# Optimization experiments

Hardware: AMD Instinct MI355X
Metric: run time of the kernel (lower is better)

The kernel has to match this reference:

```python
import jax, jax.numpy as jnp
import numpy as np

NUM_LAYERS = 10
HIDDEN = 5
INPUT = 5
SEQ = 457
OUT = 457


def _lstm_layer(x_tbi, W_ih, W_hh, b):
    # x_tbi: [T, B, in]; W_ih: [4H, in]; W_hh: [4H, H]; b: [4H] (b_ih + b_hh)
    B = x_tbi.shape[1]
    h0 = jnp.zeros((B, HIDDEN), x_tbi.dtype)
    c0 = jnp.zeros((B, HIDDEN), x_tbi.dtype)
    # precompute input projections for all timesteps: [T, B, 4H]
    xW = jnp.einsum('tbi,gi->tbg', x_tbi, W_ih) + b

    def step(carry, xw_t):
        h, c = carry
        gates = xw_t + h @ W_hh.T  # [B, 4H]
        i, f, g, o = jnp.split(gates, 4, axis=-1)  # PyTorch gate order i,f,g,o
        i = jax.nn.sigmoid(i)
        f = jax.nn.sigmoid(f)
        g = jnp.tanh(g)
        o = jax.nn.sigmoid(o)
        c = f * c + i * g
        h = o * jnp.tanh(c)
        return (h, c), h

    (_, _), hs = jax.lax.scan(step, (h0, c0), xW)
    return hs  # [T, B, H]


def setup_inputs() -> dict:
    key = jax.random.key(0)
    ks = jax.random.split(key, 8)
    B = 4096
    x = jax.random.normal(ks[0], (B, SEQ, INPUT), dtype=jnp.float32)
    attn = jnp.ones((B, SEQ), dtype=jnp.int64)
    tok = jnp.zeros((B, SEQ), dtype=jnp.int64)
    s = 1.0 / np.sqrt(HIDDEN)
    # layer 0 input size == HIDDEN, so all layers stack uniformly
    W_ih = jax.random.uniform(ks[1], (NUM_LAYERS, 4 * HIDDEN, INPUT), jnp.float32, -s, s)
    W_hh = jax.random.uniform(ks[2], (NUM_LAYERS, 4 * HIDDEN, HIDDEN), jnp.float32, -s, s)
    b_ih = jax.random.uniform(ks[3], (NUM_LAYERS, 4 * HIDDEN), jnp.float32, -s, s)
    b_hh = jax.random.uniform(ks[4], (NUM_LAYERS, 4 * HIDDEN), jnp.float32, -s, s)
    sf = 1.0 / np.sqrt(HIDDEN * SEQ)
    fc_W = jax.random.uniform(ks[5], (OUT, HIDDEN * SEQ), jnp.float32, -sf, sf)
    fc_b = jax.random.uniform(ks[6], (OUT,), jnp.float32, -sf, sf)
    return {"a_input_ids": x, "a_attention_mask": attn, "a_token_type_ids": tok,
            "W_ih": W_ih, "W_hh": W_hh, "b_ih": b_ih, "b_hh": b_hh,
            "fc_W": fc_W, "fc_b": fc_b}


def reference(a_input_ids, a_attention_mask, a_token_type_ids, W_ih, W_hh, b_ih, b_hh, fc_W, fc_b):
    x = jnp.transpose(a_input_ids.astype(jnp.float32), (1, 0, 2))  # [T, B, 5]
    b = b_ih + b_hh
    for l in range(NUM_LAYERS):
        x = _lstm_layer(x, W_ih[l], W_hh[l], b[l])  # [T, B, H]
    out = jnp.transpose(x, (1, 0, 2))  # [B, T, H]
    flat = out.reshape(out.shape[0], -1)  # [B, T*H]
    # dropout is identity at inference
    return flat @ fc_W.T + fc_b  # [B, OUT]
```

## Files before the change

### kernel.cpp

```cpp
#include <hip/hip_runtime.h>

#define NUM_LAYERS 10
#define HIDDEN 5
#define SEQ 457
#define BATCH 4096
#define OUT_DIM 457
#define KD 2285
#define KPAD 2304
#define NKT 72
#define OPAD 512

typedef __attribute__((ext_vector_type(8))) short short8;
typedef __attribute__((ext_vector_type(4))) float f32x4;

__device__ __forceinline__ float frcp(float x){ return __builtin_amdgcn_rcpf(x); }
__device__ __forceinline__ float fexp2(float x){ return __builtin_amdgcn_exp2f(x); }
__device__ __forceinline__ unsigned short f2bf(float f){
    unsigned u = __float_as_uint(f);
    u = (u + 0x7FFFu + ((u>>16)&1u)) >> 16;
    return (unsigned short)u;
}
__device__ __forceinline__ float bf2f(unsigned short h){
    return __uint_as_float(((unsigned)h) << 16);
}

#define GB 16
#define NW 11
#define CSTRIDE 20
#define SLOTB (GB*CSTRIDE)
#define BUFS (NUM_LAYERS*SLOTB)

__global__ __launch_bounds__(64*NW) void lstm_kernel(
    const float* __restrict__ x,
    const float* __restrict__ W_ih,
    const float* __restrict__ W_hh,
    const float* __restrict__ b_ih,
    const float* __restrict__ b_hh,
    unsigned short* __restrict__ Hb)
{
    __shared__ unsigned short Cs[2*BUFS];
    const int tid = threadIdx.x;
    const int wv = tid >> 6;
    const int lane = tid & 63;
    const int bBlk = blockIdx.x * GB;

    for (int i = tid; i < 2*BUFS; i += 64*NW) Cs[i] = 0;
    __syncthreads();

    const int m  = lane & 15;
    const int kg = lane >> 4;
    short8 wf0, wf1;
    f32x4 bias0, bias1;
    int off0 = 0, off1 = 0;
    float c0 = 0.f, c1 = 0.f;
    float xr[5];
    const float* xb = nullptr;

    if (wv < NUM_LAYERS) {
        const int l = wv;
        {
            const int j = m >> 2, g = m & 3;
            const float scg = (g == 2) ? 2.8853900817779268f : -1.4426950408889634f;
            const int row = l*20 + g*5 + j;
#pragma unroll
            for (int e = 0; e < 8; ++e) {
                const int k = kg*8 + e;
                unsigned short v = 0;
                if (k < 30) {
                    const int ki = (k < 10) ? k : (k < 20) ? k-10 : k-20;
                    const float w = scg * ((ki < 5) ? W_ih[row*5+ki] : W_hh[row*5+ki-5]);
                    const unsigned short hi = f2bf(w);
                    v = (k >= 20) ? f2bf(w - bf2f(hi)) : hi;
                }
                wf0[e] = (short)v;
            }
        }
        {
#pragma unroll
            for (int e = 0; e < 8; ++e) {
                unsigned short v = 0;
                if (m < 4) {
                    const int g = m;
                    const float scg = (g == 2) ? 2.8853900817779268f : -1.4426950408889634f;
                    const int row = l*20 + g*5 + 4;
                    const int k = kg*8 + e;
                    if (k < 30) {
                        const int ki = (k < 10) ? k : (k < 20) ? k-10 : k-20;
                        const float w = scg * ((ki < 5) ? W_ih[row*5+ki] : W_hh[row*5+ki-5]);
                        const unsigned short hi = f2bf(w);
                        v = (k >= 20) ? f2bf(w - bf2f(hi)) : hi;
                    }
                }
                wf1[e] = (short)v;
            }
        }
#pragma unroll
        for (int r = 0; r < 4; ++r) {
            const float scg = (r == 2) ? 2.8853900817779268f : -1.4426950408889634f;
            bias0[r] = scg * (b_ih[wv*20 + r*5 + kg] + b_hh[wv*20 + r*5 + kg]);
            bias1[r] = (kg == 0) ? scg * (b_ih[wv*20 + r*5 + 4] + b_hh[wv*20 + r*5 + 4]) : 0.f;
        }
        off0 = (kg==0) ? 0 : (kg==1) ? 16 : (kg==2) ? 32 : 8;
        off1 = (kg==0) ? 8 : (kg==1) ? 24 : (kg==2) ? 0 : 16;
    } else {
        const int b = lane & 15;
        xb = x + (size_t)(bBlk + b) * (SEQ*HIDDEN);
        for (int i = lane; i < GB*(KPAD-KD); i += 64) {
            const int bb = i / (KPAD-KD), cc = i - bb*(KPAD-KD);
            Hb[(size_t)(bBlk+bb)*KPAD + KD + cc] = 0;
        }
        if (lane < GB) {
            unsigned short* cw = &Cs[0*BUFS + 0*SLOTB + b*CSTRIDE];
#pragma unroll
            for (int i = 0; i < 5; ++i) {
                const float xv = xb[i];
                const unsigned short hi = f2bf(xv);
                cw[i] = hi;
                cw[10+i] = f2bf(xv - bf2f(hi));
            }
#pragma unroll
            for (int i = 0; i < 5; ++i) xr[i] = xb[5 + i];
        }
    }
    __syncthreads();

    for (int s = 0; s < SEQ + NUM_LAYERS - 1; ++s) {
        if (wv < NUM_LAYERS) {
            const int l = wv;
            const char* cb = (const char*)&Cs[(s&1)*BUFS + l*SLOTB + m*CSTRIDE];
            union { short8 s8; unsigned long u[2]; } bv;
            bv.u[0] = *(const unsigned long*)(cb + off0);
            bv.u[1] = *(const unsigned long*)(cb + off1);

            f32x4 d0 = __builtin_amdgcn_mfma_f32_16x16x32_bf16(wf0, bv.s8, bias0, 0, 0, 0);
            f32x4 d2 = __builtin_amdgcn_mfma_f32_16x16x32_bf16(wf1, bv.s8, bias1, 0, 0, 0);

            const float ig  = frcp(1.f + fexp2(d0[0]));
            const float fg  = frcp(1.f + fexp2(d0[1]));
            const float gg  = 1.f - 2.f*frcp(1.f + fexp2(d0[2]));
            const float og  = frcp(1.f + fexp2(d0[3]));
            const float ig1 = frcp(1.f + fexp2(d2[0]));
            const float fg1 = frcp(1.f + fexp2(d2[1]));
            const float gg1 = 1.f - 2.f*frcp(1.f + fexp2(d2[2]));
            const float og1 = frcp(1.f + fexp2(d2[3]));

            const int t = s - l;
            if (t >= 0 && t < SEQ) {
                c0 = fg*c0 + ig*gg;
                const float th0 = 1.f - 2.f*frcp(1.f + fexp2(2.8853900817779268f*c0));
                const float h0 = og*th0;
                c1 = fg1*c1 + ig1*gg1;
                const float th1 = 1.f - 2.f*frcp(1.f + fexp2(2.8853900817779268f*c1));
                const float h1 = og1*th1;

                const unsigned short h0hi = f2bf(h0);
                const unsigned short h0lo = f2bf(h0 - bf2f(h0hi));
                const unsigned short h1hi = f2bf(h1);
                const unsigned short h1lo = f2bf(h1 - bf2f(h1hi));

                unsigned short* wb = &Cs[((s+1)&1)*BUFS];
                unsigned short* myslot = wb + l*SLOTB + m*CSTRIDE;
                const int j = kg;
                myslot[5+j]  = h0hi;
                myslot[15+j] = h0lo;
                if (l < NUM_LAYERS-1) {
                    unsigned short* nx = wb + (l+1)*SLOTB + m*CSTRIDE;
                    nx[j]    = h0hi;
                    nx[10+j] = h0lo;
                    if (kg == 0) { nx[4] = h1hi; nx[14] = h1lo; }
                }
                if (kg == 0) { myslot[5+4] = h1hi; myslot[15+4] = h1lo; }
                if (l == NUM_LAYERS-1) {
                    unsigned short* hr = Hb + (size_t)(bBlk + m)*KPAD + t*5;
                    hr[j] = h0hi;
                    if (kg == 0) hr[4] = h1hi;
                }
            }
        } else {
            const int b = lane & 15;
            if (lane < GB) {
                const int tw = s + 1;
                if (tw < SEQ) {
                    unsigned short* cw = &Cs[((s+1)&1)*BUFS + 0*SLOTB + b*CSTRIDE];
#pragma unroll
                    for (int i = 0; i < 5; ++i) {
                        const unsigned short hi = f2bf(xr[i]);
                        cw[i] = hi;
                        cw[10+i] = f2bf(xr[i] - bf2f(hi));
                    }
                }
                int t2 = s + 2; if (t2 > SEQ-1) t2 = SEQ-1;
#pragma unroll
                for (int i = 0; i < 5; ++i) xr[i] = xb[t2*5 + i];
            }
        }
        __syncthreads();
    }
}

__global__ __launch_bounds__(256) void convw_kernel(
    const float* __restrict__ fcW,
    unsigned short* __restrict__ Whi,
    unsigned short* __restrict__ Wlo)
{
    const int idx = blockIdx.x * 256 + threadIdx.x;
    if (idx >= OPAD * KPAD) return;
    const int o = idx / KPAD;
    const int k = idx - o * KPAD;
    float v = 0.0f;
    if (o < OUT_DIM && k < KD) v = fcW[o * KD + k];
    const unsigned short hi = f2bf(v);
    Whi[idx] = hi;
    Wlo[idx] = f2bf(v - bf2f(hi));
}

__global__ __launch_bounds__(256) void fc_kernel(
    const unsigned short* __restrict__ Hb,
    const unsigned short* __restrict__ Whi,
    const unsigned short* __restrict__ Wlo,
    const float* __restrict__ fcb,
    float* __restrict__ out)
{
    const int lane = threadIdx.x & 63;
    const int w = threadIdx.x >> 6;
    const int b0 = blockIdx.x * 64 + w * 16;
    const int o0 = blockIdx.y * 64;
    const int row = lane & 15;
    const int kq = (lane >> 4) * 8;

    const unsigned short* Ha  = Hb  + (size_t)(b0 + row) * KPAD + kq;
    const unsigned short* Wh0 = Whi + (size_t)(o0 + row) * KPAD + kq;
    const unsigned short* Wl0 = Wlo + (size_t)(o0 + row) * KPAD + kq;

    f32x4 acc0 = {0.f,0.f,0.f,0.f}, acc1 = acc0, acc2 = acc0, acc3 = acc0;

    short8 a_c   = *(const short8*)(Ha);
    short8 wh0_c = *(const short8*)(Wh0);
    short8 wh1_c = *(const short8*)(Wh0 + 16*KPAD);
    short8 wh2_c = *(const short8*)(Wh0 + 32*KPAD);
    short8 wh3_c = *(const short8*)(Wh0 + 48*KPAD);
    short8 wl0_c = *(const short8*)(Wl0);
    short8 wl1_c = *(const short8*)(Wl0 + 16*KPAD);
    short8 wl2_c = *(const short8*)(Wl0 + 32*KPAD);
    short8 wl3_c = *(const short8*)(Wl0 + 48*KPAD);

    for (int kk = 0; kk < NKT; ++kk) {
        const int kb = (kk+1 < NKT) ? (kk+1)*32 : kk*32;
        const short8 a_n   = *(const short8*)(Ha  + kb);
        const short8 wh0_n = *(const short8*)(Wh0 + kb);
        const short8 wh1_n = *(const short8*)(Wh0 + 16*KPAD + kb);
        const short8 wh2_n = *(const short8*)(Wh0 + 32*KPAD + kb);
        const short8 wh3_n = *(const short8*)(Wh0 + 48*KPAD + kb);
        const short8 wl0_n = *(const short8*)(Wl0 + kb);
        const short8 wl1_n = *(const short8*)(Wl0 + 16*KPAD + kb);
        const short8 wl2_n = *(const short8*)(Wl0 + 32*KPAD + kb);
        const short8 wl3_n = *(const short8*)(Wl0 + 48*KPAD + kb);

        acc0 = __builtin_amdgcn_mfma_f32_16x16x32_bf16(a_c, wh0_c, acc0, 0,0,0);
        acc1 = __builtin_amdgcn_mfma_f32_16x16x32_bf16(a_c, wh1_c, acc1, 0,0,0);
        acc2 = __builtin_amdgcn_mfma_f32_16x16x32_bf16(a_c, wh2_c, acc2, 0,0,0);
        acc3 = __builtin_amdgcn_mfma_f32_16x16x32_bf16(a_c, wh3_c, acc3, 0,0,0);
        acc0 = __builtin_amdgcn_mfma_f32_16x16x32_bf16(a_c, wl0_c, acc0, 0,0,0);
        acc1 = __builtin_amdgcn_mfma_f32_16x16x32_bf16(a_c, wl1_c, acc1, 0,0,0);
        acc2 = __builtin_amdgcn_mfma_f32_16x16x32_bf16(a_c, wl2_c, acc2, 0,0,0);
        acc3 = __builtin_amdgcn_mfma_f32_16x16x32_bf16(a_c, wl3_c, acc3, 0,0,0);

        a_c = a_n;
        wh0_c = wh0_n; wh1_c = wh1_n; wh2_c = wh2_n; wh3_c = wh3_n;
        wl0_c = wl0_n; wl1_c = wl1_n; wl2_c = wl2_n; wl3_c = wl3_n;
    }

    const int ocol = lane & 15;
    const int br0 = (lane >> 4) * 4;
#pragma unroll
    for (int nb = 0; nb < 4; ++nb) {
        const int o = o0 + nb * 16 + ocol;
        if (o < OUT_DIM) {
            const float bias = fcb[o];
            const f32x4 acc = (nb == 0) ? acc0 : (nb == 1) ? acc1 : (nb == 2) ? acc2 : acc3;
#pragma unroll
            for (int r = 0; r < 4; ++r) {
                const int bi = b0 + br0 + r;
                out[(size_t)bi * OUT_DIM + o] = acc[r] + bias;
            }
        }
    }
}

extern "C" void kernel_launch(void* const* d_in, const int* in_sizes, int n_in,
                              void* d_out, int out_size, void* d_ws, size_t ws_size,
                              hipStream_t stream) {
    const float* x    = (const float*)d_in[0];
    const float* W_ih = (const float*)d_in[3];
    const float* W_hh = (const float*)d_in[4];
    const float* b_ih = (const float*)d_in[5];
    const float* b_hh = (const float*)d_in[6];
    const float* fcW  = (const float*)d_in[7];
    const float* fcb  = (const float*)d_in[8];
    float* out = (float*)d_out;

    unsigned short* Hb  = (unsigned short*)d_ws;
    unsigned short* Whi = (unsigned short*)((char*)d_ws + (size_t)BATCH * KPAD * 2);
    unsigned short* Wlo = (unsigned short*)((char*)d_ws + (size_t)BATCH * KPAD * 2 + (size_t)OPAD * KPAD * 2);

    lstm_kernel<<<dim3(BATCH / GB), dim3(64 * NW), 0, stream>>>(
        x, W_ih, W_hh, b_ih, b_hh, Hb);

    convw_kernel<<<dim3((OPAD * KPAD + 255) / 256), dim3(256), 0, stream>>>(fcW, Whi, Wlo);

    fc_kernel<<<dim3(BATCH / 64, OPAD / 64), dim3(256), 0, stream>>>(Hb, Whi, Wlo, fcb, out);
}
```

Before: 553.4 us.

## Process two timesteps per barrier in LSTM wavefront and pre-swizzle FC operands

The LSTM wavefront pipeline now stages two timesteps per shared-memory slot, so each layer wave runs two cell updates between __syncthreads. This roughly halves the number of block-wide barriers, which serialize the recurrence. The last layer's hidden states and the FC weights are now written in a tile-swizzled MFMA fragment layout, so the FC kernel reads contiguous 16-byte chunks per lane. Packed bf16 conversion via v_cvt_pk_bf16_f32 replaces scalar rounding, at the cost of more complex indexing and a larger LDS footprint.

```diff
diff --git a/kernel.cpp b/kernel.cpp
--- a/kernel.cpp
+++ b/kernel.cpp
@@ -12,23 +12,33 @@
 
 typedef __attribute__((ext_vector_type(8))) short short8;
 typedef __attribute__((ext_vector_type(4))) float f32x4;
+typedef unsigned long long ull;
+typedef unsigned short ushort;
 
 __device__ __forceinline__ float frcp(float x){ return __builtin_amdgcn_rcpf(x); }
 __device__ __forceinline__ float fexp2(float x){ return __builtin_amdgcn_exp2f(x); }
-__device__ __forceinline__ unsigned short f2bf(float f){
+__device__ __forceinline__ ushort f2bf(float f){
     unsigned u = __float_as_uint(f);
     u = (u + 0x7FFFu + ((u>>16)&1u)) >> 16;
-    return (unsigned short)u;
-}
-__device__ __forceinline__ float bf2f(unsigned short h){
-    return __uint_as_float(((unsigned)h) << 16);
-}
+    return (ushort)u;
+}
+__device__ __forceinline__ float bf2f(ushort h){ return __uint_as_float(((unsigned)h) << 16); }
+__device__ __forceinline__ unsigned cvtpk(float a, float b){
+    unsigned r;
+    asm("v_cvt_pk_bf16_f32 %0, %1, %2" : "=v"(r) : "v"(a), "v"(b));
+    return r;
+}
+__device__ __forceinline__ void act4(const f32x4 d, float& i_, float& f_, float& g_, float& o_){
+    i_ = frcp(1.f + fexp2(d[0]));
+    f_ = frcp(1.f + fexp2(d[1]));
+    g_ = 1.f - 2.f*frcp(1.f + fexp2(d[2]));
+    o_ = frcp(1.f + fexp2(d[3]));
+}
+__device__ __forceinline__ float tanhc(float c){ return 1.f - 2.f*frcp(1.f + fexp2(2.8853900817779268f*c)); }
 
 #define GB 16
 #define NW 11
-#define CSTRIDE 20
-#define SLOTB (GB*CSTRIDE)
-#define BUFS (NUM_LAYERS*SLOTB)
+#define BUFS 6400
 
 __global__ __launch_bounds__(64*NW) void lstm_kernel(
     const float* __restrict__ x,
@@ -36,28 +46,36 @@
     const float* __restrict__ W_hh,
     const float* __restrict__ b_ih,
     const float* __restrict__ b_hh,
-    unsigned short* __restrict__ Hb)
+    ushort* __restrict__ HbP)
 {
-    __shared__ unsigned short Cs[2*BUFS];
+    __shared__ ull CsQ[3200];
+    ushort* Cs = (ushort*)CsQ;
     const int tid = threadIdx.x;
-    const int wv = tid >> 6;
     const int lane = tid & 63;
-    const int bBlk = blockIdx.x * GB;
-
-    for (int i = tid; i < 2*BUFS; i += 64*NW) Cs[i] = 0;
+    const int lS = __builtin_amdgcn_readfirstlane(tid >> 6);
+    const int bg = blockIdx.x;
+    const int hbBase = bg * (NKT*512);
+
+    for (int i = tid; i < 3200; i += 64*NW) CsQ[i] = 0;
     __syncthreads();
 
     const int m  = lane & 15;
     const int kg = lane >> 4;
-    short8 wf0, wf1;
-    f32x4 bias0, bias1;
-    int off0 = 0, off1 = 0;
-    float c0 = 0.f, c1 = 0.f;
-    float xr[5];
-    const float* xb = nullptr;
-
-    if (wv < NUM_LAYERS) {
-        const int l = wv;
+
+    short8 wf0{}, wf1{};
+    f32x4 bias0{}, bias1{};
+    float c0 = 0.f, c4 = 0.f;
+    float xr0=0,xr1=0,xr2=0,xr3=0,xr4=0;
+    const float* xb2 = nullptr;
+    const int half = lane >> 4;
+    const int gb = lane & 15;
+
+    const char* rd0 = nullptr; const char* rd1 = nullptr;
+    ushort* myP = nullptr; ushort* j4P = nullptr;
+    char* gw = nullptr;
+
+    if (lS < NUM_LAYERS) {
+        const int l = lS;
         {
             const int j = m >> 2, g = m & 3;
             const float scg = (g == 2) ? 2.8853900817779268f : -1.4426950408889634f;
@@ -65,11 +83,11 @@
 #pragma unroll
             for (int e = 0; e < 8; ++e) {
                 const int k = kg*8 + e;
-                unsigned short v = 0;
+                ushort v = 0;
                 if (k < 30) {
                     const int ki = (k < 10) ? k : (k < 20) ? k-10 : k-20;
                     const float w = scg * ((ki < 5) ? W_ih[row*5+ki] : W_hh[row*5+ki-5]);
-                    const unsigned short hi = f2bf(w);
+                    const ushort hi = f2bf(w);
                     v = (k >= 20) ? f2bf(w - bf2f(hi)) : hi;
                 }
                 wf0[e] = (short)v;
@@ -78,7 +96,7 @@
         {
 #pragma unroll
             for (int e = 0; e < 8; ++e) {
-                unsigned short v = 0;
+                ushort v = 0;
                 if (m < 4) {
                     const int g = m;
                     const float scg = (g == 2) ? 2.8853900817779268f : -1.4426950408889634f;
@@ -87,7 +105,7 @@
                     if (k < 30) {
                         const int ki = (k < 10) ? k : (k < 20) ? k-10 : k-20;
                         const float w = scg * ((ki < 5) ? W_ih[row*5+ki] : W_hh[row*5+ki-5]);
-                        const unsigned short hi = f2bf(w);
+                        const ushort hi = f2bf(w);
                         v = (k >= 20) ? f2bf(w - bf2f(hi)) : hi;
                     }
                 }
@@ -97,164 +115,217 @@
 #pragma unroll
         for (int r = 0; r < 4; ++r) {
             const float scg = (r == 2) ? 2.8853900817779268f : -1.4426950408889634f;
-            bias0[r] = scg * (b_ih[wv*20 + r*5 + kg] + b_hh[wv*20 + r*5 + kg]);
-            bias1[r] = (kg == 0) ? scg * (b_ih[wv*20 + r*5 + 4] + b_hh[wv*20 + r*5 + 4]) : 0.f;
-        }
-        off0 = (kg==0) ? 0 : (kg==1) ? 16 : (kg==2) ? 32 : 8;
-        off1 = (kg==0) ? 8 : (kg==1) ? 24 : (kg==2) ? 0 : 16;
+            bias0[r] = scg * (b_ih[l*20 + r*5 + kg] + b_hh[l*20 + r*5 + kg]);
+            bias1[r] = (kg == 0) ? scg * (b_ih[l*20 + r*5 + 4] + b_hh[l*20 + r*5 + 4]) : 0.f;
+        }
+        const int off0 = (kg==0) ? 0 : (kg==1) ? 16 : (kg==2) ? 32 : 8;
+        const int off1 = (kg==0) ? 8 : (kg==1) ? 24 : (kg==2) ? 0 : 16;
+        const int slotB = (l*16 + m) * 80;
+        rd0 = (const char*)Cs + slotB + off0;
+        rd1 = (const char*)Cs + slotB + off1;
+        myP = Cs + (l*16 + m)*40 + kg;
+        j4P = Cs + (l*16 + m)*40;
     } else {
-        const int b = lane & 15;
-        xb = x + (size_t)(bBlk + b) * (SEQ*HIDDEN);
-        for (int i = lane; i < GB*(KPAD-KD); i += 64) {
-            const int bb = i / (KPAD-KD), cc = i - bb*(KPAD-KD);
-            Hb[(size_t)(bBlk+bb)*KPAD + KD + cc] = 0;
-        }
-        if (lane < GB) {
-            unsigned short* cw = &Cs[0*BUFS + 0*SLOTB + b*CSTRIDE];
-#pragma unroll
-            for (int i = 0; i < 5; ++i) {
-                const float xv = xb[i];
-                const unsigned short hi = f2bf(xv);
-                cw[i] = hi;
-                cw[10+i] = f2bf(xv - bf2f(hi));
-            }
-#pragma unroll
-            for (int i = 0; i < 5; ++i) xr[i] = xb[5 + i];
-        }
+        if (lane < 32) {
+            xb2 = x + (size_t)(bg*GB + gb) * (SEQ*HIDDEN);
+            gw = (char*)Cs + gb*80 + half*40;
+        }
+        ull* slab = (ull*)(HbP + hbBase + 71*512);
+        slab[lane] = 0; slab[lane + 64] = 0;
     }
     __syncthreads();
 
-    for (int s = 0; s < SEQ + NUM_LAYERS - 1; ++s) {
-        if (wv < NUM_LAYERS) {
-            const int l = wv;
-            const char* cb = (const char*)&Cs[(s&1)*BUFS + l*SLOTB + m*CSTRIDE];
-            union { short8 s8; unsigned long u[2]; } bv;
-            bv.u[0] = *(const unsigned long*)(cb + off0);
-            bv.u[1] = *(const unsigned long*)(cb + off1);
-
-            f32x4 d0 = __builtin_amdgcn_mfma_f32_16x16x32_bf16(wf0, bv.s8, bias0, 0, 0, 0);
-            f32x4 d2 = __builtin_amdgcn_mfma_f32_16x16x32_bf16(wf1, bv.s8, bias1, 0, 0, 0);
-
-            const float ig  = frcp(1.f + fexp2(d0[0]));
-            const float fg  = frcp(1.f + fexp2(d0[1]));
-            const float gg  = 1.f - 2.f*frcp(1.f + fexp2(d0[2]));
-            const float og  = frcp(1.f + fexp2(d0[3]));
-            const float ig1 = frcp(1.f + fexp2(d2[0]));
-            const float fg1 = frcp(1.f + fexp2(d2[1]));
-            const float gg1 = 1.f - 2.f*frcp(1.f + fexp2(d2[2]));
-            const float og1 = frcp(1.f + fexp2(d2[3]));
-
-            const int t = s - l;
-            if (t >= 0 && t < SEQ) {
-                c0 = fg*c0 + ig*gg;
-                const float th0 = 1.f - 2.f*frcp(1.f + fexp2(2.8853900817779268f*c0));
-                const float h0 = og*th0;
-                c1 = fg1*c1 + ig1*gg1;
-                const float th1 = 1.f - 2.f*frcp(1.f + fexp2(2.8853900817779268f*c1));
-                const float h1 = og1*th1;
-
-                const unsigned short h0hi = f2bf(h0);
-                const unsigned short h0lo = f2bf(h0 - bf2f(h0hi));
-                const unsigned short h1hi = f2bf(h1);
-                const unsigned short h1lo = f2bf(h1 - bf2f(h1hi));
-
-                unsigned short* wb = &Cs[((s+1)&1)*BUFS];
-                unsigned short* myslot = wb + l*SLOTB + m*CSTRIDE;
-                const int j = kg;
-                myslot[5+j]  = h0hi;
-                myslot[15+j] = h0lo;
-                if (l < NUM_LAYERS-1) {
-                    unsigned short* nx = wb + (l+1)*SLOTB + m*CSTRIDE;
-                    nx[j]    = h0hi;
-                    nx[10+j] = h0lo;
-                    if (kg == 0) { nx[4] = h1hi; nx[14] = h1lo; }
+    if (lS == NUM_LAYERS && lane < 32) {
+        float v0 = xb2[half*5+0], v1 = xb2[half*5+1], v2 = xb2[half*5+2],
+              v3 = xb2[half*5+3], v4 = xb2[half*5+4];
+        unsigned p01 = cvtpk(v0,v1), p23 = cvtpk(v2,v3);
+        ushort p4 = f2bf(v4);
+        float l0 = v0 - __uint_as_float(p01<<16), l1 = v1 - __uint_as_float(p01 & 0xFFFF0000u);
+        float l2 = v2 - __uint_as_float(p23<<16), l3 = v3 - __uint_as_float(p23 & 0xFFFF0000u);
+        float l4 = v4 - bf2f(p4);
+        unsigned q01 = cvtpk(l0,l1), q23 = cvtpk(l2,l3);
+        *(unsigned*)(gw + 0)  = p01;
+        *(unsigned*)(gw + 4)  = p23;
+        *(ushort*)  (gw + 8)  = p4;
+        *(unsigned*)(gw + 20) = q01;
+        *(unsigned*)(gw + 24) = q23;
+        *(ushort*)  (gw + 28) = f2bf(l4);
+        xr0 = xb2[(2+half)*5+0]; xr1 = xb2[(2+half)*5+1]; xr2 = xb2[(2+half)*5+2];
+        xr3 = xb2[(2+half)*5+3]; xr4 = xb2[(2+half)*5+4];
+    }
+    __syncthreads();
+
+    int s = 0;
+    auto cell = [&](int PP) {
+        const int WP = 1 - PP;
+        const int t0 = 2*(s - lS);
+        const bool a0 = (t0 >= 0) & (t0 <= SEQ-1);
+        const bool a1 = (t0 >= 0) & (t0 <  SEQ-1);
+        union { short8 v; ull q[2]; } bf;
+        bf.q[0] = *(const ull*)(rd0 + PP*12800);
+        bf.q[1] = *(const ull*)(rd1 + PP*12800);
+        f32x4 d0 = __builtin_amdgcn_mfma_f32_16x16x32_bf16(wf0, bf.v, bias0, 0,0,0);
+        f32x4 d4 = __builtin_amdgcn_mfma_f32_16x16x32_bf16(wf1, bf.v, bias1, 0,0,0);
+        float ig,fg,gg,og, i4,f4,g4,o4;
+        act4(d0, ig,fg,gg,og);
+        act4(d4, i4,f4,g4,o4);
+        if (a0) {
+            c0 = fg*c0 + ig*gg;
+            const float h = og * tanhc(c0);
+            c4 = f4*c4 + i4*g4;
+            const float h4 = o4 * tanhc(c4);
+            const unsigned ph = cvtpk(h, h4);
+            const unsigned pl = cvtpk(h - __uint_as_float(ph<<16),
+                                      h4 - __uint_as_float(ph & 0xFFFF0000u));
+            myP[PP*BUFS + 25] = (ushort)ph;
+            myP[PP*BUFS + 35] = (ushort)pl;
+            if (kg == 0) { j4P[PP*BUFS + 29] = (ushort)(ph>>16); j4P[PP*BUFS + 39] = (ushort)(pl>>16); }
+            if (lS < NUM_LAYERS-1) {
+                myP[WP*BUFS + 640] = (ushort)ph;
+                myP[WP*BUFS + 650] = (ushort)pl;
+                if (kg == 0) { j4P[WP*BUFS + 644] = (ushort)(ph>>16); j4P[WP*BUFS + 654] = (ushort)(pl>>16); }
+            } else {
+                const int k = t0*5 + kg;
+                HbP[hbBase + (k>>5)*512 + ((k>>3)&3)*128 + m*8 + (k&7)] = (ushort)ph;
+                if (kg == 0) {
+                    const int k4 = t0*5 + 4;
+                    HbP[hbBase + (k4>>5)*512 + ((k4>>3)&3)*128 + m*8 + (k4&7)] = (ushort)(ph>>16);
                 }
-                if (kg == 0) { myslot[5+4] = h1hi; myslot[15+4] = h1lo; }
-                if (l == NUM_LAYERS-1) {
-                    unsigned short* hr = Hb + (size_t)(bBlk + m)*KPAD + t*5;
-                    hr[j] = h0hi;
-                    if (kg == 0) hr[4] = h1hi;
+            }
+        }
+        bf.q[0] = *(const ull*)(rd0 + PP*12800 + 40);
+        bf.q[1] = *(const ull*)(rd1 + PP*12800 + 40);
+        d0 = __builtin_amdgcn_mfma_f32_16x16x32_bf16(wf0, bf.v, bias0, 0,0,0);
+        d4 = __builtin_amdgcn_mfma_f32_16x16x32_bf16(wf1, bf.v, bias1, 0,0,0);
+        act4(d0, ig,fg,gg,og);
+        act4(d4, i4,f4,g4,o4);
+        if (a1) {
+            c0 = fg*c0 + ig*gg;
+            const float h = og * tanhc(c0);
+            c4 = f4*c4 + i4*g4;
+            const float h4 = o4 * tanhc(c4);
+            const unsigned ph = cvtpk(h, h4);
+            const unsigned pl = cvtpk(h - __uint_as_float(ph<<16),
+                                      h4 - __uint_as_float(ph & 0xFFFF0000u));
+            myP[WP*BUFS + 5]  = (ushort)ph;
+            myP[WP*BUFS + 15] = (ushort)pl;
+            if (kg == 0) { j4P[WP*BUFS + 9] = (ushort)(ph>>16); j4P[WP*BUFS + 19] = (ushort)(pl>>16); }
+            if (lS < NUM_LAYERS-1) {
+                myP[WP*BUFS + 660] = (ushort)ph;
+                myP[WP*BUFS + 670] = (ushort)pl;
+                if (kg == 0) { j4P[WP*BUFS + 664] = (ushort)(ph>>16); j4P[WP*BUFS + 674] = (ushort)(pl>>16); }
+            } else {
+                const int k = (t0+1)*5 + kg;
+                HbP[hbBase + (k>>5)*512 + ((k>>3)&3)*128 + m*8 + (k&7)] = (ushort)ph;
+                if (kg == 0) {
+                    const int k4 = (t0+1)*5 + 4;
+                    HbP[hbBase + (k4>>5)*512 + ((k4>>3)&3)*128 + m*8 + (k4&7)] = (ushort)(ph>>16);
                 }
             }
-        } else {
-            const int b = lane & 15;
-            if (lane < GB) {
-                const int tw = s + 1;
-                if (tw < SEQ) {
-                    unsigned short* cw = &Cs[((s+1)&1)*BUFS + 0*SLOTB + b*CSTRIDE];
-#pragma unroll
-                    for (int i = 0; i < 5; ++i) {
-                        const unsigned short hi = f2bf(xr[i]);
-                        cw[i] = hi;
-                        cw[10+i] = f2bf(xr[i] - bf2f(hi));
-                    }
-                }
-                int t2 = s + 2; if (t2 > SEQ-1) t2 = SEQ-1;
-#pragma unroll
-                for (int i = 0; i < 5; ++i) xr[i] = xb[t2*5 + i];
-            }
-        }
-        __syncthreads();
+        }
+    };
+    auto ghost = [&](int PP) {
+        const int WP = 1 - PP;
+        if (lane < 32) {
+            const int tw = 2*s + 2 + half;
+            if (tw < SEQ) {
+                unsigned p01 = cvtpk(xr0,xr1), p23 = cvtpk(xr2,xr3);
+                ushort p4 = f2bf(xr4);
+                float l0 = xr0 - __uint_as_float(p01<<16), l1 = xr1 - __uint_as_float(p01 & 0xFFFF0000u);
+                float l2 = xr2 - __uint_as_float(p23<<16), l3 = xr3 - __uint_as_float(p23 & 0xFFFF0000u);
+                float l4 = xr4 - bf2f(p4);
+                unsigned q01 = cvtpk(l0,l1), q23 = cvtpk(l2,l3);
+                *(unsigned*)(gw + WP*12800 + 0)  = p01;
+                *(unsigned*)(gw + WP*12800 + 4)  = p23;
+                *(ushort*)  (gw + WP*12800 + 8)  = p4;
+                *(unsigned*)(gw + WP*12800 + 20) = q01;
+                *(unsigned*)(gw + WP*12800 + 24) = q23;
+                *(ushort*)  (gw + WP*12800 + 28) = f2bf(l4);
+            }
+            int tn = 2*s + 4 + half; if (tn > SEQ-1) tn = SEQ-1;
+            xr0 = xb2[tn*5+0]; xr1 = xb2[tn*5+1]; xr2 = xb2[tn*5+2];
+            xr3 = xb2[tn*5+3]; xr4 = xb2[tn*5+4];
+        }
+    };
+
+    for (int it = 0; it < 119; ++it) {
+        if (lS < NUM_LAYERS) cell(0); else ghost(0);
+        __syncthreads(); ++s;
+        if (lS < NUM_LAYERS) cell(1); else ghost(1);
+        __syncthreads(); ++s;
     }
 }
 
 __global__ __launch_bounds__(256) void convw_kernel(
     const float* __restrict__ fcW,
-    unsigned short* __restrict__ Whi,
-    unsigned short* __restrict__ Wlo)
+    ushort* __restrict__ WhiP,
+    ushort* __restrict__ WloP)
 {
-    const int idx = blockIdx.x * 256 + threadIdx.x;
-    if (idx >= OPAD * KPAD) return;
-    const int o = idx / KPAD;
-    const int k = idx - o * KPAD;
-    float v = 0.0f;
-    if (o < OUT_DIM && k < KD) v = fcW[o * KD + k];
-    const unsigned short hi = f2bf(v);
-    Whi[idx] = hi;
-    Wlo[idx] = f2bf(v - bf2f(hi));
+    const int tidg = blockIdx.x * 256 + threadIdx.x;
+    if (tidg >= 32*NKT*64) return;
+    const int L  = tidg & 63;
+    const int kk = (tidg >> 6) % NKT;
+    const int og = tidg / (64*NKT);
+    const int o = og*16 + (L & 15);
+    const int kb = kk*32 + ((L >> 4) << 3);
+    short8 hi8{}, lo8{};
+#pragma unroll
+    for (int e = 0; e < 8; ++e) {
+        const int k = kb + e;
+        float v = 0.f;
+        if (o < OUT_DIM && k < KD) v = fcW[(size_t)o*KD + k];
+        const ushort hi = f2bf(v);
+        hi8[e] = (short)hi;
+        lo8[e] = (short)f2bf(v - bf2f(hi));
+    }
+    *(short8*)&WhiP[(size_t)tidg*8] = hi8;
+    *(short8*)&WloP[(size_t)tidg*8] = lo8;
 }
 
 __global__ __launch_bounds__(256) void fc_kernel(
-    const unsigned short* __restrict__ Hb,
-    const unsigned short* __restrict__ Whi,
-    const unsigned short* __restrict__ Wlo,
+    const ushort* __restrict__ HbP,
+    const ushort* __restrict__ WhiP,
+    const ushort* __restrict__ WloP,
     const float* __restrict__ fcb,
     float* __restrict__ out)
 {
     const int lane = threadIdx.x & 63;
     const int w = threadIdx.x >> 6;
-    const int b0 = blockIdx.x * 64 + w * 16;
-    const int o0 = blockIdx.y * 64;
-    const int row = lane & 15;
-    const int kq = (lane >> 4) * 8;
-
-    const unsigned short* Ha  = Hb  + (size_t)(b0 + row) * KPAD + kq;
-    const unsigned short* Wh0 = Whi + (size_t)(o0 + row) * KPAD + kq;
-    const unsigned short* Wl0 = Wlo + (size_t)(o0 + row) * KPAD + kq;
-
-    f32x4 acc0 = {0.f,0.f,0.f,0.f}, acc1 = acc0, acc2 = acc0, acc3 = acc0;
-
-    short8 a_c   = *(const short8*)(Ha);
+    const int bgi = blockIdx.x*4 + w;
+    const int ogB = blockIdx.y*4;
+    const ushort* Ap  = HbP  + (size_t)bgi*(NKT*512) + lane*8;
+    const ushort* Wh0 = WhiP + (size_t)(ogB+0)*(NKT*512) + lane*8;
+    const ushort* Wh1 = WhiP + (size_t)(ogB+1)*(NKT*512) + lane*8;
+    const ushort* Wh2 = WhiP + (size_t)(ogB+2)*(NKT*512) + lane*8;
+    const ushort* Wh3 = WhiP + (size_t)(ogB+3)*(NKT*512) + lane*8;
+    const ushort* Wl0 = WloP + (size_t)(ogB+0)*(NKT*512) + lane*8;
+    const ushort* Wl1 = WloP + (size_t)(ogB+1)*(NKT*512) + lane*8;
+    const ushort* Wl2 = WloP + (size_t)(ogB+2)*(NKT*512) + lane*8;
+    const ushort* Wl3 = WloP + (size_t)(ogB+3)*(NKT*512) + lane*8;
+
+    f32x4 acc0{}, acc1{}, acc2{}, acc3{};
+
+    short8 a_c   = *(const short8*)(Ap);
     short8 wh0_c = *(const short8*)(Wh0);
-    short8 wh1_c = *(const short8*)(Wh0 + 16*KPAD);
-    short8 wh2_c = *(const short8*)(Wh0 + 32*KPAD);
-    short8 wh3_c = *(const short8*)(Wh0 + 48*KPAD);
+    short8 wh1_c = *(const short8*)(Wh1);
+    short8 wh2_c = *(const short8*)(Wh2);
+    short8 wh3_c = *(const short8*)(Wh3);
     short8 wl0_c = *(const short8*)(Wl0);
-    short8 wl1_c = *(const short8*)(Wl0 + 16*KPAD);
-    short8 wl2_c = *(const short8*)(Wl0 + 32*KPAD);
-    short8 wl3_c = *(const short8*)(Wl0 + 48*KPAD);
+    short8 wl1_c = *(const short8*)(Wl1);
+    short8 wl2_c = *(const short8*)(Wl2);
+    short8 wl3_c = *(const short8*)(Wl3);
 
     for (int kk = 0; kk < NKT; ++kk) {
-        const int kb = (kk+1 < NKT) ? (kk+1)*32 : kk*32;
-        const short8 a_n   = *(const short8*)(Ha  + kb);
+        const int kb = (kk+1 < NKT) ? (kk+1)*512 : kk*512;
+        const short8 a_n   = *(const short8*)(Ap  + kb);
         const short8 wh0_n = *(const short8*)(Wh0 + kb);
-        const short8 wh1_n = *(const short8*)(Wh0 + 16*KPAD + kb);
-        const short8 wh2_n = *(const short8*)(Wh0 + 32*KPAD + kb);
-        const short8 wh3_n = *(const short8*)(Wh0 + 48*KPAD + kb);
+        const short8 wh1_n = *(const short8*)(Wh1 + kb);
+        const short8 wh2_n = *(const short8*)(Wh2 + kb);
+        const short8 wh3_n = *(const short8*)(Wh3 + kb);
         const short8 wl0_n = *(const short8*)(Wl0 + kb);
-        const short8 wl1_n = *(const short8*)(Wl0 + 16*KPAD + kb);
-        const short8 wl2_n = *(const short8*)(Wl0 + 32*KPAD + kb);
-        const short8 wl3_n = *(const short8*)(Wl0 + 48*KPAD + kb);
+        const short8 wl1_n = *(const short8*)(Wl1 + kb);
+        const short8 wl2_n = *(const short8*)(Wl2 + kb);
+        const short8 wl3_n = *(const short8*)(Wl3 + kb);
 
         acc0 = __builtin_amdgcn_mfma_f32_16x16x32_bf16(a_c, wh0_c, acc0, 0,0,0);
         acc1 = __builtin_amdgcn_mfma_f32_16x16x32_bf16(a_c, wh1_c, acc1, 0,0,0);
@@ -272,16 +343,16 @@
 
     const int ocol = lane & 15;
     const int br0 = (lane >> 4) * 4;
+    const int b0 = bgi * 16;
 #pragma unroll
     for (int nb = 0; nb < 4; ++nb) {
-        const int o = o0 + nb * 16 + ocol;
+        const int o = (ogB + nb)*16 + ocol;
         if (o < OUT_DIM) {
             const float bias = fcb[o];
-            const f32x4 acc = (nb == 0) ? acc0 : (nb == 1) ? acc1 : (nb == 2) ? acc2 : acc3;
+            const f32x4 acc = (nb==0) ? acc0 : (nb==1) ? acc1 : (nb==2) ? acc2 : acc3;
 #pragma unroll
             for (int r = 0; r < 4; ++r) {
-                const int bi = b0 + br0 + r;
-                out[(size_t)bi * OUT_DIM + o] = acc[r] + bias;
+                out[(size_t)(b0 + br0 + r)*OUT_DIM + o] = acc[r] + bias;
             }
         }
     }
@@ -299,14 +370,14 @@
     const float* fcb  = (const float*)d_in[8];
     float* out = (float*)d_out;
 
-    unsigned short* Hb  = (unsigned short*)d_ws;
-    unsigned short* Whi = (unsigned short*)((char*)d_ws + (size_t)BATCH * KPAD * 2);
-    unsigned short* Wlo = (unsigned short*)((char*)d_ws + (size_t)BATCH * KPAD * 2 + (size_t)OPAD * KPAD * 2);
-
-    lstm_kernel<<<dim3(BATCH / GB), dim3(64 * NW), 0, stream>>>(
-        x, W_ih, W_hh, b_ih, b_hh, Hb);
-
-    convw_kernel<<<dim3((OPAD * KPAD + 255) / 256), dim3(256), 0, stream>>>(fcW, Whi, Wlo);
-
-    fc_kernel<<<dim3(BATCH / 64, OPAD / 64), dim3(256), 0, stream>>>(Hb, Whi, Wlo, fcb, out);
-}
+    ushort* HbP  = (ushort*)d_ws;
+    ushort* WhiP = (ushort*)((char*)d_ws + (size_t)256*NKT*512*2);
+    ushort* WloP = (ushort*)((char*)d_ws + (size_t)256*NKT*512*2 + (size_t)32*NKT*512*2);
+
+    lstm_kernel<<<dim3(BATCH/GB), dim3(64*NW), 0, stream>>>(
+        x, W_ih, W_hh, b_ih, b_hh, HbP);
+
+    convw_kernel<<<dim3((32*NKT*64 + 255)/256), dim3(256), 0, stream>>>(fcW, WhiP, WloP);
+
+    fc_kernel<<<dim3(64, 8), dim3(256), 0, stream>>>(HbP, WhiP, WloP, fcb, out);
+}
```

Result: faster. 488.9 us (-11.7%).
